# Optimization experiments

Hardware: AMD Instinct MI355X
Metric: run time of the kernel (lower is better)

The kernel has to match this reference:

```python
import jax, jax.numpy as jnp
import numpy as np

WAY = 5  # N_way from init


def setup_inputs() -> dict:
    key = jax.random.key(0)
    k1, k2, k3, k4 = jax.random.split(key, 4)
    N, c, h, w = 80, 2048, 16, 16
    S = 512  # shuffle_num
    x = jax.random.normal(k1, (N, c, h, w), dtype=jnp.float32)
    s_ca = jax.random.uniform(k2, (N, c, 1, 1), dtype=jnp.float32)
    # random channel indices per sample (stand-in for random.sample)
    rand_index = jax.random.randint(k3, (N, S), 0, c)
    # partner offset per sample (stand-in for random j != i)
    partner = jax.random.randint(k4, (N,), 0, N - 1)
    return {"x": x, "s_ca": s_ca, "rand_index": rand_index,
            "partner": partner, "shuffle_num": S}


def reference(x, s_ca, rand_index, partner, shuffle_num):
    N, c, h, w = x.shape
    way = WAY
    scores = s_ca.reshape(N, c)
    # per-sample top-k channels by attention score
    _, topk_idx = jax.lax.top_k(scores, shuffle_num)          # [N, S]
    # partner sample j != i (offset trick guarantees inequality)
    j = (jnp.arange(N) + 1 + partner) % N                      # [N]
    bi = jnp.arange(N)[:, None]                                # [N, 1]
    x_topk = x[bi, topk_idx]                                   # [N, S, h, w]
    x_part = x[j[:, None], rand_index]                         # [N, S, h, w]
    blend = 0.7 * x_topk + 0.3 * x_part
    # scatter blended channels back (batched gather-blend-scatter)
    aug_x = x.at[bi, topk_idx].set(blend)                      # [N, c, h, w]
    # group into (way, shot, ...) and concat original + augmented episodes
    x_r = x.reshape(way, -1, c, h, w)
    aug_r = aug_x.reshape(way, -1, c, h, w)
    out = jnp.concatenate((x_r, aug_r), axis=1)                # [way, 2*shot, c, h, w]
    s = s_ca.reshape(way, -1, c, 1, 1)
    s = jnp.concatenate((s, s), axis=1)                        # repeat(1,2,1,1,1)
    out = out * s
    return out.reshape(-1, c, h, w)                            # [2N, c, h, w]
```

## Files before the change

### kernel.cpp

```cpp
#include <hip/hip_runtime.h>

#define N_SAMP 80
#define C_CH   2048
#define HW     256
#define S_TOP  512
#define HW4    64

__global__ __launch_bounds__(256) void topk_rank_kernel(
    const float* __restrict__ s_ca, int* __restrict__ rank) {
  __shared__ unsigned long long keys[C_CH];
  const int n = blockIdx.x;
  const int tid = threadIdx.x;
  const float* row = s_ca + (size_t)n * C_CH;

  for (int i = tid; i < C_CH; i += 256) {
    unsigned int b = __float_as_uint(row[i]);
    b ^= (b & 0x80000000u) ? 0xFFFFFFFFu : 0x80000000u;
    keys[i] = ((unsigned long long)b << 11) |
              (unsigned long long)(C_CH - 1 - i);
  }
  __syncthreads();

  for (int k = 2; k <= C_CH; k <<= 1) {
    for (int j = k >> 1; j > 0; j >>= 1) {
      for (int t = tid; t < C_CH / 2; t += 256) {
        int i = ((t & ~(j - 1)) << 1) | (t & (j - 1));
        int ixj = i | j;
        bool desc = ((i & k) == 0);
        unsigned long long a = keys[i];
        unsigned long long c2 = keys[ixj];
        if ((a < c2) == desc) {
          keys[i] = c2;
          keys[ixj] = a;
        }
      }
      __syncthreads();
    }
  }

  int* rrow = rank + (size_t)n * C_CH;
  for (int i = tid; i < C_CH; i += 256) rrow[i] = -1;
  __syncthreads();
  for (int t = tid; t < S_TOP; t += 256) {
    int idx = (C_CH - 1) - (int)(keys[t] & 2047ULL);
    rrow[idx] = t;
  }
}

__global__ __launch_bounds__(256) void shuffle_out_kernel(
    const float4* __restrict__ x4, const float* __restrict__ s_ca,
    const int* __restrict__ rand_index, const int* __restrict__ partner,
    const int* __restrict__ rank, float4* __restrict__ out4) {
  const unsigned int p = blockIdx.x * 256u + threadIdx.x;
  const unsigned int m = p >> 17;
  const unsigned int r = p & 131071u;
  const unsigned int ch = r >> 6;
  const unsigned int q = r & 63u;

  const unsigned int b = m & 31u;
  const unsigned int n = ((m >> 5) << 4) | (b & 15u);
  const bool aug = (b >= 16u);

  const float s = s_ca[(size_t)n * C_CH + ch];
  float4 v = x4[((size_t)n * C_CH + ch) * HW4 + q];

  if (aug) {
    const int k = rank[(size_t)n * C_CH + ch];
    if (k >= 0) {
      int jn = (int)n + 1 + partner[n];
      if (jn >= N_SAMP) jn -= N_SAMP;
      const int pc = rand_index[(size_t)n * S_TOP + k];
      const float4 u = x4[((size_t)jn * C_CH + pc) * HW4 + q];
      v.x = 0.7f * v.x + 0.3f * u.x;
      v.y = 0.7f * v.y + 0.3f * u.y;
      v.z = 0.7f * v.z + 0.3f * u.z;
      v.w = 0.7f * v.w + 0.3f * u.w;
    }
  }

  v.x *= s; v.y *= s; v.z *= s; v.w *= s;
  out4[p] = v;
}

extern "C" void kernel_launch(void* const* d_in, const int* in_sizes, int n_in,
                              void* d_out, int out_size, void* d_ws,
                              size_t ws_size, hipStream_t stream) {
  const float* x = (const float*)d_in[0];
  const float* s_ca = (const float*)d_in[1];
  const int* rand_index = (const int*)d_in[2];
  const int* partner = (const int*)d_in[3];

  int* rank = (int*)d_ws;

  topk_rank_kernel<<<N_SAMP, 256, 0, stream>>>(s_ca, rank);

  const int nblocks = (2 * N_SAMP * C_CH * HW4) / 256;
  shuffle_out_kernel<<<nblocks, 256, 0, stream>>>(
      (const float4*)x, s_ca, rand_index, partner, rank, (float4*)d_out);
}
```

Measured before the change: 499.0 us.

## Replace per-sample bitonic sort with counting rank and write both outputs per thread

The single-block-per-sample bitonic sort is replaced by a key-building kernel plus a rank kernel where each channel counts how many keys exceed its own, spreading the top-k across 640 blocks instead of 80. The output kernel now launches one thread per input float4, reads x once, and writes both the plain and the augmented output copies. This halves the reads of x and removes the serial sort's long synchronisation chain. In exchange it does O(C^2) comparisons per sample and adds a workspace buffer for the keys.

Measured after the change: 521.4 us. 1.04x slower.

```diff
diff --git a/kernel.cpp b/kernel.cpp
--- a/kernel.cpp
+++ b/kernel.cpp
@@ -6,45 +6,27 @@
 #define S_TOP  512
 #define HW4    64
 
-__global__ __launch_bounds__(256) void topk_rank_kernel(
-    const float* __restrict__ s_ca, int* __restrict__ rank) {
-  __shared__ unsigned long long keys[C_CH];
-  const int n = blockIdx.x;
-  const int tid = threadIdx.x;
-  const float* row = s_ca + (size_t)n * C_CH;
+__global__ __launch_bounds__(256) void build_keys_kernel(
+    const float* __restrict__ s_ca, unsigned long long* __restrict__ keys) {
+  const unsigned int i = blockIdx.x * 256u + threadIdx.x;
+  unsigned int b = __float_as_uint(s_ca[i]);
+  b ^= (b & 0x80000000u) ? 0xFFFFFFFFu : 0x80000000u;
+  const unsigned int ch = i & (C_CH - 1);
+  keys[i] = ((unsigned long long)b << 11) |
+            (unsigned long long)(C_CH - 1 - ch);
+}
 
-  for (int i = tid; i < C_CH; i += 256) {
-    unsigned int b = __float_as_uint(row[i]);
-    b ^= (b & 0x80000000u) ? 0xFFFFFFFFu : 0x80000000u;
-    keys[i] = ((unsigned long long)b << 11) |
-              (unsigned long long)(C_CH - 1 - i);
-  }
-  __syncthreads();
-
-  for (int k = 2; k <= C_CH; k <<= 1) {
-    for (int j = k >> 1; j > 0; j >>= 1) {
-      for (int t = tid; t < C_CH / 2; t += 256) {
-        int i = ((t & ~(j - 1)) << 1) | (t & (j - 1));
-        int ixj = i | j;
-        bool desc = ((i & k) == 0);
-        unsigned long long a = keys[i];
-        unsigned long long c2 = keys[ixj];
-        if ((a < c2) == desc) {
-          keys[i] = c2;
-          keys[ixj] = a;
-        }
-      }
-      __syncthreads();
-    }
-  }
-
-  int* rrow = rank + (size_t)n * C_CH;
-  for (int i = tid; i < C_CH; i += 256) rrow[i] = -1;
-  __syncthreads();
-  for (int t = tid; t < S_TOP; t += 256) {
-    int idx = (C_CH - 1) - (int)(keys[t] & 2047ULL);
-    rrow[idx] = t;
-  }
+__global__ __launch_bounds__(256) void rank_kernel(
+    const unsigned long long* __restrict__ keys, int* __restrict__ rank) {
+  const unsigned int bx = blockIdx.x;
+  const unsigned int n = bx >> 3;
+  const unsigned int ch = ((bx & 7u) << 8) | threadIdx.x;
+  const unsigned long long* __restrict__ krow = keys + (size_t)n * C_CH;
+  const unsigned long long u = krow[ch];
+  int cnt = 0;
+#pragma unroll 8
+  for (int kk = 0; kk < C_CH; ++kk) cnt += (krow[kk] > u) ? 1 : 0;
+  rank[(size_t)n * C_CH + ch] = (cnt < S_TOP) ? cnt : -1;
 }
 
 __global__ __launch_bounds__(256) void shuffle_out_kernel(
@@ -52,34 +34,35 @@
     const int* __restrict__ rand_index, const int* __restrict__ partner,
     const int* __restrict__ rank, float4* __restrict__ out4) {
   const unsigned int p = blockIdx.x * 256u + threadIdx.x;
-  const unsigned int m = p >> 17;
-  const unsigned int r = p & 131071u;
-  const unsigned int ch = r >> 6;
-  const unsigned int q = r & 63u;
+  const unsigned int n = p >> 17;
+  const unsigned int ch = (p >> 6) & (C_CH - 1);
+  const unsigned int q = p & 63u;
 
-  const unsigned int b = m & 31u;
-  const unsigned int n = ((m >> 5) << 4) | (b & 15u);
-  const bool aug = (b >= 16u);
+  const unsigned int g = n >> 4;
+  const unsigned int b = n & 15u;
 
   const float s = s_ca[(size_t)n * C_CH + ch];
-  float4 v = x4[((size_t)n * C_CH + ch) * HW4 + q];
+  const float4 v = x4[p];
 
-  if (aug) {
-    const int k = rank[(size_t)n * C_CH + ch];
-    if (k >= 0) {
-      int jn = (int)n + 1 + partner[n];
-      if (jn >= N_SAMP) jn -= N_SAMP;
-      const int pc = rand_index[(size_t)n * S_TOP + k];
-      const float4 u = x4[((size_t)jn * C_CH + pc) * HW4 + q];
-      v.x = 0.7f * v.x + 0.3f * u.x;
-      v.y = 0.7f * v.y + 0.3f * u.y;
-      v.z = 0.7f * v.z + 0.3f * u.z;
-      v.w = 0.7f * v.w + 0.3f * u.w;
-    }
+  const size_t plain_idx = (((size_t)(g * 32u + b) * C_CH + ch) << 6) | q;
+  float4 pv;
+  pv.x = v.x * s; pv.y = v.y * s; pv.z = v.z * s; pv.w = v.w * s;
+  out4[plain_idx] = pv;
+
+  float4 av = v;
+  const int k = rank[(size_t)n * C_CH + ch];
+  if (k >= 0) {
+    int jn = (int)n + 1 + partner[n];
+    if (jn >= N_SAMP) jn -= N_SAMP;
+    const int pc = rand_index[(size_t)n * S_TOP + k];
+    const float4 u = x4[(((size_t)jn * C_CH + pc) << 6) | q];
+    av.x = 0.7f * v.x + 0.3f * u.x;
+    av.y = 0.7f * v.y + 0.3f * u.y;
+    av.z = 0.7f * v.z + 0.3f * u.z;
+    av.w = 0.7f * v.w + 0.3f * u.w;
   }
-
-  v.x *= s; v.y *= s; v.z *= s; v.w *= s;
-  out4[p] = v;
+  av.x *= s; av.y *= s; av.z *= s; av.w *= s;
+  out4[plain_idx + (size_t)16 * C_CH * HW4] = av;
 }
 
 extern "C" void kernel_launch(void* const* d_in, const int* in_sizes, int n_in,
@@ -90,11 +73,13 @@
   const int* rand_index = (const int*)d_in[2];
   const int* partner = (const int*)d_in[3];
 
-  int* rank = (int*)d_ws;
+  unsigned long long* keys = (unsigned long long*)d_ws;
+  int* rank = (int*)((char*)d_ws + (size_t)N_SAMP * C_CH * 8);
 
-  topk_rank_kernel<<<N_SAMP, 256, 0, stream>>>(s_ca, rank);
+  build_keys_kernel<<<(N_SAMP * C_CH) / 256, 256, 0, stream>>>(s_ca, keys);
+  rank_kernel<<<N_SAMP * 8, 256, 0, stream>>>(keys, rank);
 
-  const int nblocks = (2 * N_SAMP * C_CH * HW4) / 256;
+  const int nblocks = (N_SAMP * C_CH * HW4) / 256;
   shuffle_out_kernel<<<nblocks, 256, 0, stream>>>(
       (const float4*)x, s_ca, rand_index, partner, rank, (float4*)d_out);
 }
```
